# Optimization experiments

Hardware: AMD Instinct MI355X
Metric: run time of the kernel (lower is better)

## Reference

```python
import jax, jax.numpy as jnp
import numpy as np

HIDDEN = 1024
INTER = 4096
N_EXPERTS = 8
TOP_K = 2


def setup_inputs() -> dict:
    key = jax.random.key(0)
    ks = jax.random.split(key, 5)
    B, S = 2, 1024
    scale_h = 1.0 / np.sqrt(HIDDEN)
    scale_i = 1.0 / np.sqrt(INTER)
    return {
        "hidden_states": jax.random.normal(ks[0], (B, S, HIDDEN), dtype=jnp.float32),
        "router_w": jax.random.normal(ks[1], (N_EXPERTS, HIDDEN), dtype=jnp.float32) * scale_h,
        "gate_w": jax.random.normal(ks[2], (N_EXPERTS, INTER, HIDDEN), dtype=jnp.float32) * scale_h,
        "up_w": jax.random.normal(ks[3], (N_EXPERTS, INTER, HIDDEN), dtype=jnp.float32) * scale_h,
        "down_w": jax.random.normal(ks[4], (N_EXPERTS, HIDDEN, INTER), dtype=jnp.float32) * scale_i,
        "top_k": TOP_K,
    }


def reference(hidden_states, router_w, gate_w, up_w, down_w, top_k):
    B, S, D = hidden_states.shape
    E = router_w.shape[0]
    x = hidden_states.reshape(-1, D)              # [T, D]
    T = x.shape[0]

    router_logits = x @ router_w.T                # [T, E]
    probs = jax.nn.softmax(router_logits.astype(jnp.float32), axis=-1)
    routing_weights, selected = jax.lax.top_k(probs, top_k)   # [T, k]
    routing_weights = routing_weights.astype(x.dtype)

    # Dense combine weights: w[t, e] = routing weight if expert e selected for token t else 0
    combine = jnp.zeros((T, E), x.dtype).at[jnp.arange(T)[:, None], selected].add(routing_weights)

    # SwiGLU expert MLPs, computed for all experts then combined (same math as gather/scatter loop)
    g = jnp.einsum('td,ehd->eth', x, gate_w)      # [E, T, H]
    u = jnp.einsum('td,ehd->eth', x, up_w)        # [E, T, H]
    h = jax.nn.silu(g) * u
    expert_out = jnp.einsum('eth,edh->etd', h, down_w)  # [E, T, D]
    out = jnp.einsum('etd,te->td', expert_out, combine)  # [T, D]

    return out.reshape(B, S, D), router_logits
```

## Files before the change

### kernel.cpp

```cpp
#include <hip/hip_runtime.h>
#include <hip/hip_bf16.h>

#define HIDDEN 1024
#define INTER 4096
#define NEXP 8
#define T_TOK 2048

typedef short bf16x8 __attribute__((ext_vector_type(8)));
typedef float f32x4 __attribute__((ext_vector_type(4)));

__device__ __forceinline__ unsigned short f2bf(float f) {
    union { float f; unsigned int u; } v; v.f = f;
    unsigned int u = v.u;
    unsigned int r = (u + 0x7FFFu + ((u >> 16) & 1u)) >> 16;
    return (unsigned short)r;
}

__device__ __forceinline__ uint2 pack4trunc(float4 v) {
    union { float4 f; unsigned short s[8]; } u; u.f = v;
    uint2 r;
    r.x = (unsigned int)u.s[1] | ((unsigned int)u.s[3] << 16);
    r.y = (unsigned int)u.s[5] | ((unsigned int)u.s[7] << 16);
    return r;
}

__device__ __forceinline__ void block_sync() {
    asm volatile("s_waitcnt lgkmcnt(0)" ::: "memory");
    __builtin_amdgcn_s_barrier();
    asm volatile("" ::: "memory");
}

__global__ void router_kernel(const float* __restrict__ x,
                              const float* __restrict__ rw,
                              float* __restrict__ logits_out,
                              int* __restrict__ counts,
                              int* __restrict__ ids,
                              float* __restrict__ wts) {
    int t = blockIdx.x * 4 + (threadIdx.x >> 6);
    int lane = threadIdx.x & 63;
    if (t >= T_TOK) return;
    const float4* xr = (const float4*)(x + (size_t)t * HIDDEN);
    float acc[NEXP];
#pragma unroll
    for (int e = 0; e < NEXP; e++) acc[e] = 0.f;
#pragma unroll
    for (int c = 0; c < 4; c++) {
        float4 xv = xr[lane + c * 64];
#pragma unroll
        for (int e = 0; e < NEXP; e++) {
            float4 wv = ((const float4*)(rw + (size_t)e * HIDDEN))[lane + c * 64];
            acc[e] += xv.x * wv.x + xv.y * wv.y + xv.z * wv.z + xv.w * wv.w;
        }
    }
#pragma unroll
    for (int e = 0; e < NEXP; e++) {
        float v = acc[e];
        for (int off = 32; off >= 1; off >>= 1) v += __shfl_xor(v, off, 64);
        acc[e] = v;
    }
    if (lane == 0) {
        float* lo = logits_out + (size_t)t * NEXP;
        float mx = acc[0];
#pragma unroll
        for (int e = 1; e < NEXP; e++) mx = fmaxf(mx, acc[e]);
        float p[NEXP], s = 0.f;
#pragma unroll
        for (int e = 0; e < NEXP; e++) { p[e] = __expf(acc[e] - mx); s += p[e]; }
        float inv = 1.f / s;
#pragma unroll
        for (int e = 0; e < NEXP; e++) { p[e] *= inv; lo[e] = acc[e]; }
        int i1 = 0;
#pragma unroll
        for (int e = 1; e < NEXP; e++) if (p[e] > p[i1]) i1 = e;
        int i2 = (i1 == 0) ? 1 : 0;
#pragma unroll
        for (int e = 0; e < NEXP; e++) if (e != i1 && e != i2 && p[e] > p[i2]) i2 = e;
        int s1 = atomicAdd(&counts[i1], 1);
        ids[i1 * T_TOK + s1] = t; wts[i1 * T_TOK + s1] = p[i1];
        int s2 = atomicAdd(&counts[i2], 1);
        ids[i2 * T_TOK + s2] = t; wts[i2 * T_TOK + s2] = p[i2];
    }
}

__global__ void scan_kernel(const int* __restrict__ counts, int* __restrict__ offsets) {
    if (threadIdx.x == 0) {
        int s = 0;
        for (int e = 0; e < NEXP; e++) { offsets[e] = s; s += counts[e]; }
    }
}

__global__ __launch_bounds__(1024) void gemm_gu(
    const float* __restrict__ x, const float* __restrict__ gw, const float* __restrict__ uw,
    const int* __restrict__ counts, const int* __restrict__ offsets,
    const int* __restrict__ ids, unsigned short* __restrict__ h) {
    const int e = blockIdx.z;
    const int cnt = counts[e];
    const int mt = blockIdx.y;
    if (mt * 256 >= cnt) return;
    const int nt = blockIdx.x;
    const int tid = threadIdx.x;
    const int lane = tid & 63, wid = tid >> 6;
    const int wm = wid >> 2, wn = wid & 3;

    __shared__ __align__(16) char lds[65536];

    const float* gbase = gw + (size_t)e * INTER * HIDDEN;
    const float* ubase = uw + (size_t)e * INTER * HIDDEN;

    unsigned int aoff[2], wA[2];
#pragma unroll
    for (int j = 0; j < 2; j++) {
        int idx = j * 1024 + tid;
        int row = idx >> 3, c4 = idx & 7;
        int li = mt * 256 + row; if (li >= cnt) li = cnt - 1;
        int gid = ids[e * T_TOK + li];
        aoff[j] = (unsigned int)(gid * HIDDEN + c4 * 4);
        wA[j] = (unsigned int)((c4 >> 1) * 4096 + row * 16 + (c4 & 1) * 8);
    }
    unsigned int boff, wB;
    {
        int row = tid >> 3, c4 = tid & 7;
        boff = (unsigned int)((nt * 128 + row) * HIDDEN + c4 * 4);
        wB = (unsigned int)((c4 >> 1) * 2048 + row * 16 + (c4 & 1) * 8);
    }

    f32x4 accg[4][2], accu[4][2];
#pragma unroll
    for (int mf = 0; mf < 4; mf++)
#pragma unroll
        for (int nf = 0; nf < 2; nf++)
#pragma unroll
            for (int v = 0; v < 4; v++) { accg[mf][nf][v] = 0.f; accu[mf][nf][v] = 0.f; }

    float4 av[2], gv, uv;
    av[0] = *(const float4*)(x + aoff[0]);
    av[1] = *(const float4*)(x + aoff[1]);
    gv = *(const float4*)(gbase + boff);
    uv = *(const float4*)(ubase + boff);

    for (int kt = 0; kt < 32; kt++) {
        const unsigned int bb = (unsigned int)(kt & 1) << 15;
        *(uint2*)(lds + bb + wA[0]) = pack4trunc(av[0]);
        *(uint2*)(lds + bb + wA[1]) = pack4trunc(av[1]);
        *(uint2*)(lds + bb + 16384 + wB) = pack4trunc(gv);
        *(uint2*)(lds + bb + 24576 + wB) = pack4trunc(uv);
        if (kt < 31) {
            const int ko = (kt + 1) * 32;
            av[0] = *(const float4*)(x + aoff[0] + ko);
            av[1] = *(const float4*)(x + aoff[1] + ko);
            gv = *(const float4*)(gbase + boff + ko);
            uv = *(const float4*)(ubase + boff + ko);
        }
        block_sync();
        const unsigned int kq = (unsigned int)(lane >> 4);
        bf16x8 bg[2], bu[2];
#pragma unroll
        for (int nf = 0; nf < 2; nf++) {
            unsigned int rowb = (unsigned int)(wn * 32 + nf * 16 + (lane & 15));
            bg[nf] = *(const bf16x8*)(lds + bb + 16384 + kq * 2048 + rowb * 16);
            bu[nf] = *(const bf16x8*)(lds + bb + 24576 + kq * 2048 + rowb * 16);
        }
#pragma unroll
        for (int mf = 0; mf < 4; mf++) {
            unsigned int rowa = (unsigned int)(wm * 64 + mf * 16 + (lane & 15));
            bf16x8 a = *(const bf16x8*)(lds + bb + kq * 4096 + rowa * 16);
#pragma unroll
            for (int nf = 0; nf < 2; nf++) {
                accg[mf][nf] = __builtin_amdgcn_mfma_f32_16x16x32_bf16(a, bg[nf], accg[mf][nf], 0, 0, 0);
                accu[mf][nf] = __builtin_amdgcn_mfma_f32_16x16x32_bf16(a, bu[nf], accu[mf][nf], 0, 0, 0);
            }
        }
    }

    const int hoff = offsets[e];
#pragma unroll
    for (int mf = 0; mf < 4; mf++)
#pragma unroll
        for (int v = 0; v < 4; v++) {
            int il = wm * 64 + mf * 16 + ((lane >> 4) << 2) + v;
            int i = mt * 256 + il;
            if (i < cnt) {
                size_t rowbase = (size_t)(hoff + i) * INTER + nt * 128 + wn * 32 + (lane & 15);
#pragma unroll
                for (int nf = 0; nf < 2; nf++) {
                    float g = accg[mf][nf][v], u = accu[mf][nf][v];
                    float sg = g / (1.f + __expf(-g));
                    h[rowbase + nf * 16] = f2bf(sg * u);
                }
            }
        }
}

__global__ __launch_bounds__(1024) void gemm_down(
    const unsigned short* __restrict__ h, const float* __restrict__ dw,
    const int* __restrict__ counts, const int* __restrict__ offsets,
    const int* __restrict__ ids, const float* __restrict__ wts,
    float* __restrict__ out) {
    const int ez = blockIdx.z;
    const int e = ez >> 2, ksp = ez & 3;
    const int cnt = counts[e];
    const int mt = blockIdx.y;
    if (mt * 256 >= cnt) return;
    const int nt = blockIdx.x;
    const int tid = threadIdx.x;
    const int lane = tid & 63, wid = tid >> 6;
    const int wm = wid >> 2, wn = wid & 3;

    __shared__ __align__(16) char lds[65536];

    const int hoff = offsets[e];
    const float* dbase = dw + (size_t)e * HIDDEN * INTER;

    unsigned int aoff, wAo;
    {
        int row = tid >> 2, c8 = tid & 3;
        int li = mt * 256 + row; if (li >= cnt) li = cnt - 1;
        aoff = (unsigned int)((hoff + li) * INTER + ksp * 1024 + c8 * 8);
        wAo = (unsigned int)(c8 * 4096 + row * 16);
    }
    unsigned int boff[2], wB[2];
#pragma unroll
    for (int j = 0; j < 2; j++) {
        int idx = j * 1024 + tid;
        int row = idx >> 3, c4 = idx & 7;
        boff[j] = (unsigned int)((nt * 256 + row) * INTER + ksp * 1024 + c4 * 4);
        wB[j] = (unsigned int)(16384 + (c4 >> 1) * 4096 + row * 16 + (c4 & 1) * 8);
    }

    f32x4 acc[4][4];
#pragma unroll
    for (int mf = 0; mf < 4; mf++)
#pragma unroll
        for (int nf = 0; nf < 4; nf++)
#pragma unroll
            for (int v = 0; v < 4; v++) acc[mf][nf][v] = 0.f;

    int4 avv; float4 bv[2];
    avv = *(const int4*)(h + aoff);
    bv[0] = *(const float4*)(dbase + boff[0]);
    bv[1] = *(const float4*)(dbase + boff[1]);

    for (int kt = 0; kt < 32; kt++) {
        const unsigned int bb = (unsigned int)(kt & 1) << 15;
        *(int4*)(lds + bb + wAo) = avv;
        *(uint2*)(lds + bb + wB[0]) = pack4trunc(bv[0]);
        *(uint2*)(lds + bb + wB[1]) = pack4trunc(bv[1]);
        if (kt < 31) {
            const int ko = (kt + 1) * 32;
            avv = *(const int4*)(h + aoff + ko);
            bv[0] = *(const float4*)(dbase + boff[0] + ko);
            bv[1] = *(const float4*)(dbase + boff[1] + ko);
        }
        block_sync();
        const unsigned int kq = (unsigned int)(lane >> 4);
        bf16x8 bf[4];
#pragma unroll
        for (int nf = 0; nf < 4; nf++) {
            unsigned int rowb = (unsigned int)(wn * 64 + nf * 16 + (lane & 15));
            bf[nf] = *(const bf16x8*)(lds + bb + 16384 + kq * 4096 + rowb * 16);
        }
#pragma unroll
        for (int mf = 0; mf < 4; mf++) {
            unsigned int rowa = (unsigned int)(wm * 64 + mf * 16 + (lane & 15));
            bf16x8 a = *(const bf16x8*)(lds + bb + kq * 4096 + rowa * 16);
#pragma unroll
            for (int nf = 0; nf < 4; nf++)
                acc[mf][nf] = __builtin_amdgcn_mfma_f32_16x16x32_bf16(a, bf[nf], acc[mf][nf], 0, 0, 0);
        }
    }

#pragma unroll
    for (int mf = 0; mf < 4; mf++)
#pragma unroll
        for (int v = 0; v < 4; v++) {
            int il = wm * 64 + mf * 16 + ((lane >> 4) << 2) + v;
            int i = mt * 256 + il;
            if (i < cnt) {
                int t = ids[e * T_TOK + i];
                float w = wts[e * T_TOK + i];
                float* orow = out + (size_t)t * HIDDEN + nt * 256 + wn * 64 + (lane & 15);
#pragma unroll
                for (int nf = 0; nf < 4; nf++)
                    atomicAdd(orow + nf * 16, w * acc[mf][nf][v]);
            }
        }
}

extern "C" void kernel_launch(void* const* d_in, const int* in_sizes, int n_in,
                              void* d_out, int out_size, void* d_ws, size_t ws_size,
                              hipStream_t stream) {
    const float* x  = (const float*)d_in[0];
    const float* rw = (const float*)d_in[1];
    const float* gw = (const float*)d_in[2];
    const float* uw = (const float*)d_in[3];
    const float* dw = (const float*)d_in[4];
    float* out = (float*)d_out;
    float* logits = out + (size_t)T_TOK * HIDDEN;

    int* counts  = (int*)d_ws;
    int* offsets = counts + 8;
    int* ids     = (int*)((char*)d_ws + 64);
    float* wts   = (float*)((char*)d_ws + 64 + 8 * T_TOK * 4);
    unsigned short* h = (unsigned short*)((char*)d_ws + 262144);

    hipMemsetAsync(out, 0, (size_t)T_TOK * HIDDEN * sizeof(float), stream);
    hipMemsetAsync(counts, 0, 8 * sizeof(int), stream);

    router_kernel<<<T_TOK / 4, 256, 0, stream>>>(x, rw, logits, counts, ids, wts);
    scan_kernel<<<1, 64, 0, stream>>>(counts, offsets);
    gemm_gu<<<dim3(INTER / 128, 8, NEXP), 1024, 0, stream>>>(x, gw, uw, counts, offsets, ids, h);
    gemm_down<<<dim3(HIDDEN / 256, 8, NEXP * 4), 1024, 0, stream>>>(h, dw, counts, offsets, ids, wts, out);
}
```

Before: 366.3 us.

## Replace atomic scatter in down GEMM with partial buffers and combine kernel

The down-projection GEMM no longer scatters into the output with float atomics. It now writes routing-weighted partial results into a per-expert, per-k-split buffer. The router records each token's two slot positions, and a new combine kernel gathers and sums the four partial rows per token, so the output memset is no longer needed. The down GEMM also moves to 128x128 tiles with 512 threads and a 2-way K split instead of 4-way. This removes atomic contention and the zero-fill, at the cost of an extra kernel launch plus a write and read of the partial buffer.

```diff
diff --git a/kernel.cpp b/kernel.cpp
--- a/kernel.cpp
+++ b/kernel.cpp
@@ -35,7 +35,8 @@
                               float* __restrict__ logits_out,
                               int* __restrict__ counts,
                               int* __restrict__ ids,
-                              float* __restrict__ wts) {
+                              float* __restrict__ wts,
+                              int* __restrict__ tsel) {
     int t = blockIdx.x * 4 + (threadIdx.x >> 6);
     int lane = threadIdx.x & 63;
     if (t >= T_TOK) return;
@@ -79,6 +80,8 @@
         ids[i1 * T_TOK + s1] = t; wts[i1 * T_TOK + s1] = p[i1];
         int s2 = atomicAdd(&counts[i2], 1);
         ids[i2 * T_TOK + s2] = t; wts[i2 * T_TOK + s2] = p[i2];
+        tsel[t * 2]     = i1 * T_TOK + s1;
+        tsel[t * 2 + 1] = i2 * T_TOK + s2;
     }
 }
 
@@ -110,8 +113,8 @@
     unsigned int aoff[2], wA[2];
 #pragma unroll
     for (int j = 0; j < 2; j++) {
-        int idx = j * 1024 + tid;
-        int row = idx >> 3, c4 = idx & 7;
+        int fi = j * 1024 + tid;
+        int row = fi >> 3, c4 = fi & 7;
         int li = mt * 256 + row; if (li >= cnt) li = cnt - 1;
         int gid = ids[e * T_TOK + li];
         aoff[j] = (unsigned int)(gid * HIDDEN + c4 * 4);
@@ -191,80 +194,79 @@
         }
 }
 
-__global__ __launch_bounds__(1024) void gemm_down(
+__global__ __launch_bounds__(512) void gemm_down(
     const unsigned short* __restrict__ h, const float* __restrict__ dw,
     const int* __restrict__ counts, const int* __restrict__ offsets,
-    const int* __restrict__ ids, const float* __restrict__ wts,
-    float* __restrict__ out) {
+    const float* __restrict__ wts, float* __restrict__ y) {
     const int ez = blockIdx.z;
-    const int e = ez >> 2, ksp = ez & 3;
+    const int e = ez >> 1, ksp = ez & 1;
     const int cnt = counts[e];
     const int mt = blockIdx.y;
-    if (mt * 256 >= cnt) return;
+    if (mt * 128 >= cnt) return;
     const int nt = blockIdx.x;
     const int tid = threadIdx.x;
     const int lane = tid & 63, wid = tid >> 6;
     const int wm = wid >> 2, wn = wid & 3;
 
-    __shared__ __align__(16) char lds[65536];
+    __shared__ __align__(16) char lds[32768];
 
     const int hoff = offsets[e];
     const float* dbase = dw + (size_t)e * HIDDEN * INTER;
 
     unsigned int aoff, wAo;
     {
-        int row = tid >> 2, c8 = tid & 3;
-        int li = mt * 256 + row; if (li >= cnt) li = cnt - 1;
-        aoff = (unsigned int)((hoff + li) * INTER + ksp * 1024 + c8 * 8);
-        wAo = (unsigned int)(c8 * 4096 + row * 16);
+        int row = tid >> 2, c16 = tid & 3;
+        int li = mt * 128 + row; if (li >= cnt) li = cnt - 1;
+        aoff = (unsigned int)((hoff + li) * INTER + ksp * 2048 + c16 * 8);
+        wAo = (unsigned int)(c16 * 2048 + row * 16);
     }
     unsigned int boff[2], wB[2];
 #pragma unroll
     for (int j = 0; j < 2; j++) {
-        int idx = j * 1024 + tid;
-        int row = idx >> 3, c4 = idx & 7;
-        boff[j] = (unsigned int)((nt * 256 + row) * INTER + ksp * 1024 + c4 * 4);
-        wB[j] = (unsigned int)(16384 + (c4 >> 1) * 4096 + row * 16 + (c4 & 1) * 8);
-    }
-
-    f32x4 acc[4][4];
+        int fi = j * 512 + tid;
+        int row = fi >> 3, c4 = fi & 7;
+        boff[j] = (unsigned int)((nt * 128 + row) * INTER + ksp * 2048 + c4 * 4);
+        wB[j] = (unsigned int)(8192 + (c4 >> 1) * 2048 + row * 16 + (c4 & 1) * 8);
+    }
+
+    f32x4 acc[4][2];
 #pragma unroll
     for (int mf = 0; mf < 4; mf++)
 #pragma unroll
-        for (int nf = 0; nf < 4; nf++)
+        for (int nf = 0; nf < 2; nf++)
 #pragma unroll
             for (int v = 0; v < 4; v++) acc[mf][nf][v] = 0.f;
 
-    int4 avv; float4 bv[2];
-    avv = *(const int4*)(h + aoff);
+    int4 av; float4 bv[2];
+    av = *(const int4*)(h + aoff);
     bv[0] = *(const float4*)(dbase + boff[0]);
     bv[1] = *(const float4*)(dbase + boff[1]);
 
-    for (int kt = 0; kt < 32; kt++) {
-        const unsigned int bb = (unsigned int)(kt & 1) << 15;
-        *(int4*)(lds + bb + wAo) = avv;
+    for (int kt = 0; kt < 64; kt++) {
+        const unsigned int bb = (unsigned int)(kt & 1) << 14;
+        *(int4*)(lds + bb + wAo) = av;
         *(uint2*)(lds + bb + wB[0]) = pack4trunc(bv[0]);
         *(uint2*)(lds + bb + wB[1]) = pack4trunc(bv[1]);
-        if (kt < 31) {
+        if (kt < 63) {
             const int ko = (kt + 1) * 32;
-            avv = *(const int4*)(h + aoff + ko);
+            av = *(const int4*)(h + aoff + ko);
             bv[0] = *(const float4*)(dbase + boff[0] + ko);
             bv[1] = *(const float4*)(dbase + boff[1] + ko);
         }
         block_sync();
         const unsigned int kq = (unsigned int)(lane >> 4);
-        bf16x8 bf[4];
-#pragma unroll
-        for (int nf = 0; nf < 4; nf++) {
-            unsigned int rowb = (unsigned int)(wn * 64 + nf * 16 + (lane & 15));
-            bf[nf] = *(const bf16x8*)(lds + bb + 16384 + kq * 4096 + rowb * 16);
+        bf16x8 bf[2];
+#pragma unroll
+        for (int nf = 0; nf < 2; nf++) {
+            unsigned int rowb = (unsigned int)(wn * 32 + nf * 16 + (lane & 15));
+            bf[nf] = *(const bf16x8*)(lds + bb + 8192 + kq * 2048 + rowb * 16);
         }
 #pragma unroll
         for (int mf = 0; mf < 4; mf++) {
             unsigned int rowa = (unsigned int)(wm * 64 + mf * 16 + (lane & 15));
-            bf16x8 a = *(const bf16x8*)(lds + bb + kq * 4096 + rowa * 16);
-#pragma unroll
-            for (int nf = 0; nf < 4; nf++)
+            bf16x8 a = *(const bf16x8*)(lds + bb + kq * 2048 + rowa * 16);
+#pragma unroll
+            for (int nf = 0; nf < 2; nf++)
                 acc[mf][nf] = __builtin_amdgcn_mfma_f32_16x16x32_bf16(a, bf[nf], acc[mf][nf], 0, 0, 0);
         }
     }
@@ -274,16 +276,36 @@
 #pragma unroll
         for (int v = 0; v < 4; v++) {
             int il = wm * 64 + mf * 16 + ((lane >> 4) << 2) + v;
-            int i = mt * 256 + il;
+            int i = mt * 128 + il;
             if (i < cnt) {
-                int t = ids[e * T_TOK + i];
                 float w = wts[e * T_TOK + i];
-                float* orow = out + (size_t)t * HIDDEN + nt * 256 + wn * 64 + (lane & 15);
-#pragma unroll
-                for (int nf = 0; nf < 4; nf++)
-                    atomicAdd(orow + nf * 16, w * acc[mf][nf][v]);
+                float* yrow = y + ((size_t)ksp * 4096 + hoff + i) * HIDDEN
+                                + nt * 128 + wn * 32 + (lane & 15);
+#pragma unroll
+                for (int nf = 0; nf < 2; nf++)
+                    yrow[nf * 16] = w * acc[mf][nf][v];
             }
         }
+}
+
+__global__ __launch_bounds__(256) void combine_kernel(
+    const float* __restrict__ y, const int* __restrict__ offsets,
+    const int* __restrict__ tsel, float* __restrict__ out) {
+    const int t = blockIdx.x;
+    const int d = threadIdx.x * 4;
+    int p0 = tsel[t * 2], p1 = tsel[t * 2 + 1];
+    size_t g0 = (size_t)(offsets[p0 >> 11] + (p0 & (T_TOK - 1)));
+    size_t g1 = (size_t)(offsets[p1 >> 11] + (p1 & (T_TOK - 1)));
+    float4 a0 = *(const float4*)(y + g0 * HIDDEN + d);
+    float4 a1 = *(const float4*)(y + (4096 + g0) * HIDDEN + d);
+    float4 b0 = *(const float4*)(y + g1 * HIDDEN + d);
+    float4 b1 = *(const float4*)(y + (4096 + g1) * HIDDEN + d);
+    float4 o;
+    o.x = (a0.x + a1.x) + (b0.x + b1.x);
+    o.y = (a0.y + a1.y) + (b0.y + b1.y);
+    o.z = (a0.z + a1.z) + (b0.z + b1.z);
+    o.w = (a0.w + a1.w) + (b0.w + b1.w);
+    *(float4*)(out + (size_t)t * HIDDEN + d) = o;
 }
 
 extern "C" void kernel_launch(void* const* d_in, const int* in_sizes, int n_in,
@@ -297,17 +319,20 @@
     float* out = (float*)d_out;
     float* logits = out + (size_t)T_TOK * HIDDEN;
 
-    int* counts  = (int*)d_ws;
-    int* offsets = counts + 8;
-    int* ids     = (int*)((char*)d_ws + 64);
-    float* wts   = (float*)((char*)d_ws + 64 + 8 * T_TOK * 4);
-    unsigned short* h = (unsigned short*)((char*)d_ws + 262144);
-
-    hipMemsetAsync(out, 0, (size_t)T_TOK * HIDDEN * sizeof(float), stream);
+    char* ws = (char*)d_ws;
+    int*   counts  = (int*)ws;
+    int*   offsets = (int*)(ws + 32);
+    int*   tsel    = (int*)(ws + 1024);
+    int*   ids     = (int*)(ws + 20480);
+    float* wts     = (float*)(ws + 90112);
+    unsigned short* h = (unsigned short*)(ws + 262144);
+    float* y       = (float*)(ws + 262144 + 33554432);
+
     hipMemsetAsync(counts, 0, 8 * sizeof(int), stream);
 
-    router_kernel<<<T_TOK / 4, 256, 0, stream>>>(x, rw, logits, counts, ids, wts);
+    router_kernel<<<T_TOK / 4, 256, 0, stream>>>(x, rw, logits, counts, ids, wts, tsel);
     scan_kernel<<<1, 64, 0, stream>>>(counts, offsets);
     gemm_gu<<<dim3(INTER / 128, 8, NEXP), 1024, 0, stream>>>(x, gw, uw, counts, offsets, ids, h);
-    gemm_down<<<dim3(HIDDEN / 256, 8, NEXP * 4), 1024, 0, stream>>>(h, dw, counts, offsets, ids, wts, out);
-}
+    gemm_down<<<dim3(HIDDEN / 128, 16, NEXP * 2), 512, 0, stream>>>(h, dw, counts, offsets, wts, y);
+    combine_kernel<<<T_TOK, 256, 0, stream>>>(y, offsets, tsel, out);
+}
```

Result: faster. 293.7 us (-19.8%).
